# Performance work log

Measured on AMD Instinct MI355X. Metric: run time of the kernel, lower is better.

Reference implementation:

```python
import jax, jax.numpy as jnp
import numpy as np

N_NODES = 100000
N_EDGES = 1600000
IN_DIM, HID_DIM, OUT_DIM = 64, 64, 32


def setup_inputs() -> dict:
    key = jax.random.key(0)
    ks = jax.random.split(key, 8)
    s_in = 1.0 / np.sqrt(IN_DIM)
    s_hid = 1.0 / np.sqrt(HID_DIM)
    return {
        "x": jax.random.normal(ks[0], (N_NODES, IN_DIM), dtype=jnp.float32),
        "edge_index": jax.random.randint(ks[1], (2, N_EDGES), 0, N_NODES, dtype=jnp.int64),
        "W1l": jax.random.uniform(ks[2], (IN_DIM, HID_DIM), jnp.float32, -s_in, s_in),
        "b1l": jnp.zeros((HID_DIM,), jnp.float32),
        "W1r": jax.random.uniform(ks[3], (IN_DIM, HID_DIM), jnp.float32, -s_in, s_in),
        "W2l": jax.random.uniform(ks[4], (HID_DIM, OUT_DIM), jnp.float32, -s_hid, s_hid),
        "b2l": jnp.zeros((OUT_DIM,), jnp.float32),
        "W2r": jax.random.uniform(ks[5], (HID_DIM, OUT_DIM), jnp.float32, -s_hid, s_hid),
    }


def sage_conv(x, src, dst, W_l, b_l, W_r, n_nodes):
    # PyG SAGEConv (aggr='mean'): lin_l(mean of neighbor msgs) + lin_r(x)
    msg = x[src]                                                    # [E, d] gather
    agg = jax.ops.segment_sum(msg, dst, num_segments=n_nodes)      # [N, d] scatter-add
    deg = jax.ops.segment_sum(jnp.ones_like(dst, dtype=x.dtype), dst,
                              num_segments=n_nodes)
    agg = agg / jnp.maximum(deg, 1.0)[:, None]                     # mean (0 for isolated)
    return agg @ W_l + b_l + x @ W_r


def reference(x, edge_index, W1l, b1l, W1r, W2l, b2l, W2r):
    src, dst = edge_index[0], edge_index[1]
    n = x.shape[0]
    h = jax.nn.relu(sage_conv(x, src, dst, W1l, b1l, W1r, n))
    return sage_conv(h, src, dst, W2l, b2l, W2r, n)
```

## Files before the change

### kernel.cpp

```cpp
#include <hip/hip_runtime.h>

#define N_NODES 100000
#define N_EDGES 1600000
#define B2_SHIFT 9
#define BUCK_N (1 << B2_SHIFT)
#define NB2 ((N_NODES + BUCK_N - 1) >> B2_SHIFT)
#define BCAP 9216
#define PAIR_EPB 4096
#define PAIR_BLOCKS ((N_EDGES + PAIR_EPB - 1) / PAIR_EPB)

typedef __attribute__((ext_vector_type(8))) short bf16x8;
typedef __attribute__((ext_vector_type(4))) float f32x4;

__device__ __forceinline__ unsigned pack2(float a, float b) {
    unsigned ua = __float_as_uint(a), ub = __float_as_uint(b);
    ua = (ua + 0x7FFFu + ((ua >> 16) & 1u)) >> 16;
    ub = (ub + 0x7FFFu + ((ub >> 16) & 1u)) >> 16;
    return ua | (ub << 16);
}
__device__ __forceinline__ float lo16(unsigned u) { return __uint_as_float(u << 16); }
__device__ __forceinline__ float hi16(unsigned u) { return __uint_as_float(u & 0xFFFF0000u); }

__global__ __launch_bounds__(256) void k_cast(const float* __restrict__ x,
                                              unsigned* __restrict__ xh)
{
    int i = blockIdx.x * 256 + threadIdx.x;
    if (i < N_NODES * 32) {
        float2 v = ((const float2*)x)[i];
        xh[i] = pack2(v.x, v.y);
    }
}

__global__ __launch_bounds__(256) void k_initcur(int* __restrict__ bcur)
{
    if (threadIdx.x < NB2) bcur[threadIdx.x] = threadIdx.x * BCAP;
}

__global__ __launch_bounds__(256) void k_pairs(const int* __restrict__ ei,
                                               int* __restrict__ bcur,
                                               int* __restrict__ pairs)
{
    __shared__ int lh[2][NB2];
    __shared__ int lb[2][NB2];
    for (int i = threadIdx.x; i < NB2; i += 256) { lh[0][i] = 0; lh[1][i] = 0; }
    __syncthreads();
    int cp = (threadIdx.x >> 6) & 1;
    int base = blockIdx.x * PAIR_EPB;
    int myb[16], myr[16], myp[16];
#pragma unroll
    for (int t = 0; t < 16; t++) {
        int e = base + t * 256 + threadIdx.x;
        myb[t] = -1;
        if (e < N_EDGES) {
            int dst = ei[N_EDGES + e];
            int b = dst >> B2_SHIFT;
            myb[t] = b;
            myr[t] = atomicAdd(&lh[cp][b], 1);
            myp[t] = (ei[e] << B2_SHIFT) | (dst & (BUCK_N - 1));
        }
    }
    __syncthreads();
    for (int i = threadIdx.x; i < NB2; i += 256) {
        int c0 = lh[0][i], c1 = lh[1][i];
        int basei = (c0 + c1) ? atomicAdd(&bcur[i], c0 + c1) : 0;
        lb[0][i] = basei;
        lb[1][i] = basei + c0;
    }
    __syncthreads();
#pragma unroll
    for (int t = 0; t < 16; t++) {
        if (myb[t] >= 0) {
            int slot = lb[cp][myb[t]] + myr[t];
            if (slot < (myb[t] + 1) * BCAP)
                pairs[slot] = myp[t];
        }
    }
}

__global__ __launch_bounds__(512) void k_sortb(const int* __restrict__ bcur,
                                               const int* __restrict__ pairs,
                                               int* __restrict__ sorted_src,
                                               int* __restrict__ rs,
                                               int* __restrict__ re)
{
    __shared__ int lcnt[BUCK_N];
    __shared__ int wtot[8];
    int b = blockIdx.x;
    int beg = b * BCAP, end = bcur[b];
    lcnt[threadIdx.x] = 0;
    __syncthreads();
    for (int i = beg + threadIdx.x; i < end; i += 512)
        atomicAdd(&lcnt[pairs[i] & (BUCK_N - 1)], 1);
    __syncthreads();
    int v = lcnt[threadIdx.x];
    int lane = threadIdx.x & 63, wid = threadIdx.x >> 6;
    int s = v;
#pragma unroll
    for (int off = 1; off < 64; off <<= 1) {
        int t = __shfl_up(s, off);
        if (lane >= off) s += t;
    }
    if (lane == 63) wtot[wid] = s;
    __syncthreads();
    int woff = 0;
#pragma unroll
    for (int k = 0; k < 8; k++) woff += (k < wid) ? wtot[k] : 0;
    int excl = woff + s - v;
    int n = (b << B2_SHIFT) + threadIdx.x;
    if (n < N_NODES) { rs[n] = beg + excl; re[n] = beg + excl + v; }
    __syncthreads();
    lcnt[threadIdx.x] = beg + excl;
    __syncthreads();
    for (int i = beg + threadIdx.x; i < end; i += 512) {
        int p = pairs[i];
        int idx = atomicAdd(&lcnt[p & (BUCK_N - 1)], 1);
        sorted_src[idx] = p >> B2_SHIFT;
    }
}

__global__ __launch_bounds__(256) void k_agg1(const int* __restrict__ rs,
                                              const int* __restrict__ re,
                                              const int* __restrict__ sorted_src,
                                              const unsigned* __restrict__ xh,
                                              unsigned* __restrict__ agg1h)
{
    int node = blockIdx.x * 8 + (threadIdx.x >> 5);
    if (node >= N_NODES) return;
    int d2 = threadIdx.x & 31;
    int beg = rs[node], end = re[node];
    float a0 = 0.f, a1 = 0.f, b0 = 0.f, b1 = 0.f;
    int idx = beg;
    for (; idx + 8 <= end; idx += 8) {
        int s0 = sorted_src[idx + 0], s1 = sorted_src[idx + 1];
        int s2 = sorted_src[idx + 2], s3 = sorted_src[idx + 3];
        int s4 = sorted_src[idx + 4], s5 = sorted_src[idx + 5];
        int s6 = sorted_src[idx + 6], s7 = sorted_src[idx + 7];
        unsigned p0 = xh[(size_t)s0 * 32 + d2];
        unsigned p1 = xh[(size_t)s1 * 32 + d2];
        unsigned p2 = xh[(size_t)s2 * 32 + d2];
        unsigned p3 = xh[(size_t)s3 * 32 + d2];
        unsigned p4 = xh[(size_t)s4 * 32 + d2];
        unsigned p5 = xh[(size_t)s5 * 32 + d2];
        unsigned p6 = xh[(size_t)s6 * 32 + d2];
        unsigned p7 = xh[(size_t)s7 * 32 + d2];
        a0 += lo16(p0) + lo16(p1);  a1 += hi16(p0) + hi16(p1);
        b0 += lo16(p2) + lo16(p3);  b1 += hi16(p2) + hi16(p3);
        a0 += lo16(p4) + lo16(p5);  a1 += hi16(p4) + hi16(p5);
        b0 += lo16(p6) + lo16(p7);  b1 += hi16(p6) + hi16(p7);
    }
    for (; idx + 2 <= end; idx += 2) {
        int s0 = sorted_src[idx], s1 = sorted_src[idx + 1];
        unsigned p0 = xh[(size_t)s0 * 32 + d2];
        unsigned p1 = xh[(size_t)s1 * 32 + d2];
        a0 += lo16(p0) + lo16(p1);  a1 += hi16(p0) + hi16(p1);
    }
    if (idx < end) {
        unsigned p = xh[(size_t)sorted_src[idx] * 32 + d2];
        a0 += lo16(p);  a1 += hi16(p);
    }
    agg1h[(size_t)node * 32 + d2] = pack2(a0 + b0, a1 + b1);
}

#define TPW 2
#define NTILE ((N_NODES + 15) / 16)
#define NODE_BLOCKS (((NTILE + TPW - 1) / TPW + 3) / 4)
__global__ __launch_bounds__(256) void k_node_mfma(
    const unsigned* __restrict__ xh, const unsigned* __restrict__ agg1h,
    const int* __restrict__ rs, const int* __restrict__ re,
    const float* __restrict__ W1l, const float* __restrict__ b1l,
    const float* __restrict__ W1r, const float* __restrict__ W2l,
    const float* __restrict__ W2r,
    unsigned* __restrict__ t2h, float* __restrict__ t3)
{
    __shared__ uint4 sWF[24 * 64];
    __shared__ float sH[4][16 * 68];
    __shared__ float sT[4][16 * 44];

    for (int s = threadIdx.x; s < 1536; s += 256) {
        int f = s >> 6, l = s & 63;
        int m = l & 15, q = l >> 4;
        float w[8];
        if (f < 16) {
            int jt = f >> 2, ks = f & 3;
            int j = jt * 16 + m;
            int k0 = ks * 32 + q * 8;
#pragma unroll
            for (int i = 0; i < 8; i++) {
                int kk = k0 + i;
                w[i] = (kk < 64) ? W1l[kk * 64 + j] : W1r[(kk - 64) * 64 + j];
            }
        } else {
            int f2 = f - 16;
            int jt = f2 >> 1, ks = f2 & 1;
            int j = jt * 16 + m;
            int k0 = ks * 32 + q * 8;
#pragma unroll
            for (int i = 0; i < 8; i++) {
                int kk = k0 + i;
                w[i] = (j < 32) ? W2l[kk * 32 + j] : W2r[kk * 32 + (j - 32)];
            }
        }
        sWF[f * 64 + l] = make_uint4(pack2(w[0], w[1]), pack2(w[2], w[3]),
                                     pack2(w[4], w[5]), pack2(w[6], w[7]));
    }
    __syncthreads();

    int w = threadIdx.x >> 6, lane = threadIdx.x & 63;
    int m = lane & 15, q = lane >> 4;

    bf16x8 WF1[4][4], WF2[4][2];
#pragma unroll
    for (int jt = 0; jt < 4; jt++) {
#pragma unroll
        for (int ks = 0; ks < 4; ks++)
            WF1[jt][ks] = __builtin_bit_cast(bf16x8, sWF[(jt * 4 + ks) * 64 + lane]);
#pragma unroll
        for (int ks = 0; ks < 2; ks++)
            WF2[jt][ks] = __builtin_bit_cast(bf16x8, sWF[(16 + jt * 2 + ks) * 64 + lane]);
    }
    float bias[4];
#pragma unroll
    for (int jt = 0; jt < 4; jt++) bias[jt] = b1l[jt * 16 + m];

    float* myH = &sH[w][0];
    float* myT = &sT[w][0];
    int gw = blockIdx.x * 4 + w;

    for (int t = 0; t < TPW; t++) {
        int tile = gw * TPW + t;
        if (tile >= NTILE) break;
        int nb = tile * 16;

        int nc = nb + m; if (nc >= N_NODES) nc = N_NODES - 1;
        const uint4* arow = (const uint4*)(agg1h + (size_t)nc * 32);
        const uint4* xrow = (const uint4*)(xh + (size_t)nc * 32);
        bf16x8 AM[2], AX[2];
        AM[0] = __builtin_bit_cast(bf16x8, arow[q]);
        AM[1] = __builtin_bit_cast(bf16x8, arow[4 + q]);
        AX[0] = __builtin_bit_cast(bf16x8, xrow[q]);
        AX[1] = __builtin_bit_cast(bf16x8, xrow[4 + q]);

        float invr[4];
#pragma unroll
        for (int r = 0; r < 4; r++) {
            int nn = nb + q * 4 + r;
            int nc2 = (nn < N_NODES) ? nn : 0;
            invr[r] = 1.0f / fmaxf((float)(re[nc2] - rs[nc2]), 1.0f);
        }

#pragma unroll
        for (int jt = 0; jt < 4; jt++) {
            f32x4 aM = {0.f, 0.f, 0.f, 0.f}, aX = {0.f, 0.f, 0.f, 0.f};
            aM = __builtin_amdgcn_mfma_f32_16x16x32_bf16(AM[0], WF1[jt][0], aM, 0, 0, 0);
            aM = __builtin_amdgcn_mfma_f32_16x16x32_bf16(AM[1], WF1[jt][1], aM, 0, 0, 0);
            aX = __builtin_amdgcn_mfma_f32_16x16x32_bf16(AX[0], WF1[jt][2], aX, 0, 0, 0);
            aX = __builtin_amdgcn_mfma_f32_16x16x32_bf16(AX[1], WF1[jt][3], aX, 0, 0, 0);
#pragma unroll
            for (int r = 0; r < 4; r++) {
                float hv = fmaxf(aM[r] * invr[r] + aX[r] + bias[jt], 0.0f);
                myH[(q * 4 + r) * 68 + jt * 16 + m] = hv;
            }
        }

        bf16x8 A2[2];
#pragma unroll
        for (int ks = 0; ks < 2; ks++) {
            const float* p = &myH[m * 68 + ks * 32 + q * 8];
            float4 v0 = *(const float4*)p;
            float4 v1 = *(const float4*)(p + 4);
            uint4 u = make_uint4(pack2(v0.x, v0.y), pack2(v0.z, v0.w),
                                 pack2(v1.x, v1.y), pack2(v1.z, v1.w));
            A2[ks] = __builtin_bit_cast(bf16x8, u);
        }

#pragma unroll
        for (int jt = 0; jt < 4; jt++) {
            f32x4 acc = {0.f, 0.f, 0.f, 0.f};
            acc = __builtin_amdgcn_mfma_f32_16x16x32_bf16(A2[0], WF2[jt][0], acc, 0, 0, 0);
            acc = __builtin_amdgcn_mfma_f32_16x16x32_bf16(A2[1], WF2[jt][1], acc, 0, 0, 0);
            if (jt < 2) {
#pragma unroll
                for (int r = 0; r < 4; r++)
                    myT[(q * 4 + r) * 44 + jt * 16 + m] = acc[r];
            } else {
#pragma unroll
                for (int r = 0; r < 4; r++) {
                    int nn = nb + q * 4 + r;
                    if (nn < N_NODES)
                        t3[(size_t)nn * 32 + (jt - 2) * 16 + m] = acc[r];
                }
            }
        }

        int ni = lane >> 2, u4g = lane & 3;
        const float* tp = &myT[ni * 44 + u4g * 8];
        float4 a = *(const float4*)tp;
        float4 b = *(const float4*)(tp + 4);
        if (nb + ni < N_NODES) {
            uint4 o = make_uint4(pack2(a.x, a.y), pack2(a.z, a.w),
                                 pack2(b.x, b.y), pack2(b.z, b.w));
            *(uint4*)(t2h + (size_t)(nb + ni) * 16 + u4g * 4) = o;
        }
    }
}

__global__ __launch_bounds__(256) void k_agg2out(
    const int* __restrict__ rs, const int* __restrict__ re,
    const int* __restrict__ sorted_src,
    const unsigned* __restrict__ t2h, const float* __restrict__ t3,
    const float* __restrict__ b2l, float* __restrict__ out)
{
    int node = blockIdx.x * 16 + (threadIdx.x >> 4);
    if (node >= N_NODES) return;
    int d2 = threadIdx.x & 15;
    int beg = rs[node], end = re[node];
    float a0 = 0.f, a1 = 0.f, b0 = 0.f, b1 = 0.f;
    int idx = beg;
    for (; idx + 8 <= end; idx += 8) {
        int s0 = sorted_src[idx + 0], s1 = sorted_src[idx + 1];
        int s2 = sorted_src[idx + 2], s3 = sorted_src[idx + 3];
        int s4 = sorted_src[idx + 4], s5 = sorted_src[idx + 5];
        int s6 = sorted_src[idx + 6], s7 = sorted_src[idx + 7];
        unsigned p0 = t2h[(size_t)s0 * 16 + d2];
        unsigned p1 = t2h[(size_t)s1 * 16 + d2];
        unsigned p2 = t2h[(size_t)s2 * 16 + d2];
        unsigned p3 = t2h[(size_t)s3 * 16 + d2];
        unsigned p4 = t2h[(size_t)s4 * 16 + d2];
        unsigned p5 = t2h[(size_t)s5 * 16 + d2];
        unsigned p6 = t2h[(size_t)s6 * 16 + d2];
        unsigned p7 = t2h[(size_t)s7 * 16 + d2];
        a0 += lo16(p0) + lo16(p1);  a1 += hi16(p0) + hi16(p1);
        b0 += lo16(p2) + lo16(p3);  b1 += hi16(p2) + hi16(p3);
        a0 += lo16(p4) + lo16(p5);  a1 += hi16(p4) + hi16(p5);
        b0 += lo16(p6) + lo16(p7);  b1 += hi16(p6) + hi16(p7);
    }
    for (; idx + 2 <= end; idx += 2) {
        int s0 = sorted_src[idx], s1 = sorted_src[idx + 1];
        unsigned p0 = t2h[(size_t)s0 * 16 + d2];
        unsigned p1 = t2h[(size_t)s1 * 16 + d2];
        a0 += lo16(p0) + lo16(p1);  a1 += hi16(p0) + hi16(p1);
    }
    if (idx < end) {
        unsigned p = t2h[(size_t)sorted_src[idx] * 16 + d2];
        a0 += lo16(p);  a1 += hi16(p);
    }
    float inv = 1.0f / fmaxf((float)(end - beg), 1.0f);
    float2 tv = ((const float2*)(t3 + (size_t)node * 32))[d2];
    float2 bv = ((const float2*)b2l)[d2];
    ((float2*)(out + (size_t)node * 32))[d2] =
        make_float2((a0 + b0) * inv + tv.x + bv.x,
                    (a1 + b1) * inv + tv.y + bv.y);
}

extern "C" void kernel_launch(void* const* d_in, const int* in_sizes, int n_in,
                              void* d_out, int out_size, void* d_ws, size_t ws_size,
                              hipStream_t stream) {
    const float* x   = (const float*)d_in[0];
    const int*   ei  = (const int*)d_in[1];
    const float* W1l = (const float*)d_in[2];
    const float* b1l = (const float*)d_in[3];
    const float* W1r = (const float*)d_in[4];
    const float* W2l = (const float*)d_in[5];
    const float* b2l = (const float*)d_in[6];
    const float* W2r = (const float*)d_in[7];
    float* out = (float*)d_out;

    const size_t N = N_NODES;
    int* wsi = (int*)d_ws;
    int*      pairs      = wsi;
    int*      sorted_src = wsi + 1806336;
    int*      bcur       = wsi + 3612672;
    int*      rs         = wsi + 3612928;
    int*      re         = wsi + 3712928;
    unsigned* xh         = (unsigned*)(wsi + 3812928);
    unsigned* t2h        = xh + 32 * N;
    unsigned* agg1h      = t2h + 16 * N;
    float*    t3         = (float*)(agg1h + 32 * N);

    k_cast   <<<(int)((N * 32 + 255) / 256), 256, 0, stream>>>(x, xh);
    k_initcur<<<1, 256, 0, stream>>>(bcur);
    k_pairs  <<<PAIR_BLOCKS, 256, 0, stream>>>(ei, bcur, pairs);
    k_sortb  <<<NB2, 512, 0, stream>>>(bcur, pairs, sorted_src, rs, re);

    k_agg1     <<<(int)((N + 7) / 8), 256, 0, stream>>>(rs, re, sorted_src, xh, agg1h);
    k_node_mfma<<<NODE_BLOCKS, 256, 0, stream>>>(xh, agg1h, rs, re,
                                                 W1l, b1l, W1r, W2l, W2r, t2h, t3);
    k_agg2out  <<<(int)((N + 15) / 16), 256, 0, stream>>>(rs, re, sorted_src,
                                                 t2h, t3, b2l, out);
}
```

Measured before the change: 209.1 us.

## Fuse cast, bucket init, pair binning and weight packing into one prep kernel

Merges the x-to-bf16 cast, bucket-counter init, edge pair binning and bf16 weight-fragment packing into a single kernel launch whose blocks pick a role from blockIdx. The bucket cursors are reset with a memset and now hold relative offsets. The node MFMA kernel copies prepacked weights from global memory instead of each block re-packing them. The sort kernel stages each bucket's pairs in shared memory so it reads global memory once, and the cast is vectorised to float4. This aims to cut launch count and redundant per-block weight packing, at the cost of a larger shared-memory footprint in the sort kernel.

```diff
diff --git a/kernel.cpp b/kernel.cpp
--- a/kernel.cpp
+++ b/kernel.cpp
@@ -8,6 +8,8 @@
 #define BCAP 9216
 #define PAIR_EPB 4096
 #define PAIR_BLOCKS ((N_EDGES + PAIR_EPB - 1) / PAIR_EPB)
+#define CAST_BLOCKS 6250
+#define PREP_BLOCKS (PAIR_BLOCKS + 1 + CAST_BLOCKS)
 
 typedef __attribute__((ext_vector_type(8))) short bf16x8;
 typedef __attribute__((ext_vector_type(4))) float f32x4;
@@ -21,58 +23,83 @@
 __device__ __forceinline__ float lo16(unsigned u) { return __uint_as_float(u << 16); }
 __device__ __forceinline__ float hi16(unsigned u) { return __uint_as_float(u & 0xFFFF0000u); }
 
-__global__ __launch_bounds__(256) void k_cast(const float* __restrict__ x,
-                                              unsigned* __restrict__ xh)
-{
-    int i = blockIdx.x * 256 + threadIdx.x;
-    if (i < N_NODES * 32) {
-        float2 v = ((const float2*)x)[i];
-        xh[i] = pack2(v.x, v.y);
-    }
-}
-
-__global__ __launch_bounds__(256) void k_initcur(int* __restrict__ bcur)
-{
-    if (threadIdx.x < NB2) bcur[threadIdx.x] = threadIdx.x * BCAP;
-}
-
-__global__ __launch_bounds__(256) void k_pairs(const int* __restrict__ ei,
-                                               int* __restrict__ bcur,
-                                               int* __restrict__ pairs)
+__global__ __launch_bounds__(256) void k_prep(
+    const float* __restrict__ x, const int* __restrict__ ei,
+    const float* __restrict__ W1l, const float* __restrict__ W1r,
+    const float* __restrict__ W2l, const float* __restrict__ W2r,
+    unsigned* __restrict__ xh, int* __restrict__ bcur,
+    int* __restrict__ pairs, uint4* __restrict__ wf)
 {
     __shared__ int lh[2][NB2];
     __shared__ int lb[2][NB2];
-    for (int i = threadIdx.x; i < NB2; i += 256) { lh[0][i] = 0; lh[1][i] = 0; }
-    __syncthreads();
-    int cp = (threadIdx.x >> 6) & 1;
-    int base = blockIdx.x * PAIR_EPB;
-    int myb[16], myr[16], myp[16];
-#pragma unroll
-    for (int t = 0; t < 16; t++) {
-        int e = base + t * 256 + threadIdx.x;
-        myb[t] = -1;
-        if (e < N_EDGES) {
-            int dst = ei[N_EDGES + e];
-            int b = dst >> B2_SHIFT;
-            myb[t] = b;
-            myr[t] = atomicAdd(&lh[cp][b], 1);
-            myp[t] = (ei[e] << B2_SHIFT) | (dst & (BUCK_N - 1));
-        }
-    }
-    __syncthreads();
-    for (int i = threadIdx.x; i < NB2; i += 256) {
-        int c0 = lh[0][i], c1 = lh[1][i];
-        int basei = (c0 + c1) ? atomicAdd(&bcur[i], c0 + c1) : 0;
-        lb[0][i] = basei;
-        lb[1][i] = basei + c0;
-    }
-    __syncthreads();
-#pragma unroll
-    for (int t = 0; t < 16; t++) {
-        if (myb[t] >= 0) {
-            int slot = lb[cp][myb[t]] + myr[t];
-            if (slot < (myb[t] + 1) * BCAP)
-                pairs[slot] = myp[t];
+
+    if (blockIdx.x < PAIR_BLOCKS) {
+        for (int i = threadIdx.x; i < NB2; i += 256) { lh[0][i] = 0; lh[1][i] = 0; }
+        __syncthreads();
+        int cp = (threadIdx.x >> 6) & 1;
+        int base = blockIdx.x * PAIR_EPB;
+        int myb[16], myr[16], myp[16];
+#pragma unroll
+        for (int t = 0; t < 16; t++) {
+            int e = base + t * 256 + threadIdx.x;
+            myb[t] = -1;
+            if (e < N_EDGES) {
+                int dst = ei[N_EDGES + e];
+                int b = dst >> B2_SHIFT;
+                myb[t] = b;
+                myr[t] = atomicAdd(&lh[cp][b], 1);
+                myp[t] = (ei[e] << B2_SHIFT) | (dst & (BUCK_N - 1));
+            }
+        }
+        __syncthreads();
+        for (int i = threadIdx.x; i < NB2; i += 256) {
+            int c0 = lh[0][i], c1 = lh[1][i];
+            int basei = (c0 + c1) ? atomicAdd(&bcur[i], c0 + c1) : 0;
+            lb[0][i] = basei;
+            lb[1][i] = basei + c0;
+        }
+        __syncthreads();
+#pragma unroll
+        for (int t = 0; t < 16; t++) {
+            if (myb[t] >= 0) {
+                int slot = lb[cp][myb[t]] + myr[t];
+                if (slot < BCAP)
+                    pairs[myb[t] * BCAP + slot] = myp[t];
+            }
+        }
+    } else if (blockIdx.x == PAIR_BLOCKS) {
+        for (int s = threadIdx.x; s < 1536; s += 256) {
+            int f = s >> 6, l = s & 63;
+            int m = l & 15, q = l >> 4;
+            float w[8];
+            if (f < 16) {
+                int jt = f >> 2, ks = f & 3;
+                int j = jt * 16 + m;
+                int k0 = ks * 32 + q * 8;
+#pragma unroll
+                for (int i = 0; i < 8; i++) {
+                    int kk = k0 + i;
+                    w[i] = (kk < 64) ? W1l[kk * 64 + j] : W1r[(kk - 64) * 64 + j];
+                }
+            } else {
+                int f2 = f - 16;
+                int jt = f2 >> 1, ks = f2 & 1;
+                int j = jt * 16 + m;
+                int k0 = ks * 32 + q * 8;
+#pragma unroll
+                for (int i = 0; i < 8; i++) {
+                    int kk = k0 + i;
+                    w[i] = (j < 32) ? W2l[kk * 32 + j] : W2r[kk * 32 + (j - 32)];
+                }
+            }
+            wf[s] = make_uint4(pack2(w[0], w[1]), pack2(w[2], w[3]),
+                               pack2(w[4], w[5]), pack2(w[6], w[7]));
+        }
+    } else {
+        int i = (blockIdx.x - PAIR_BLOCKS - 1) * 256 + threadIdx.x;
+        if (i < N_NODES * 16) {
+            float4 v = ((const float4*)x)[i];
+            ((uint2*)xh)[i] = make_uint2(pack2(v.x, v.y), pack2(v.z, v.w));
         }
     }
 }
@@ -83,14 +110,18 @@
                                                int* __restrict__ rs,
                                                int* __restrict__ re)
 {
+    __shared__ int sp[BCAP];
     __shared__ int lcnt[BUCK_N];
     __shared__ int wtot[8];
     int b = blockIdx.x;
-    int beg = b * BCAP, end = bcur[b];
+    int beg = b * BCAP;
+    int cnt = bcur[b];
+    if (cnt > BCAP) cnt = BCAP;
+    for (int i = threadIdx.x; i < cnt; i += 512) sp[i] = pairs[beg + i];
     lcnt[threadIdx.x] = 0;
     __syncthreads();
-    for (int i = beg + threadIdx.x; i < end; i += 512)
-        atomicAdd(&lcnt[pairs[i] & (BUCK_N - 1)], 1);
+    for (int i = threadIdx.x; i < cnt; i += 512)
+        atomicAdd(&lcnt[sp[i] & (BUCK_N - 1)], 1);
     __syncthreads();
     int v = lcnt[threadIdx.x];
     int lane = threadIdx.x & 63, wid = threadIdx.x >> 6;
@@ -111,8 +142,8 @@
     __syncthreads();
     lcnt[threadIdx.x] = beg + excl;
     __syncthreads();
-    for (int i = beg + threadIdx.x; i < end; i += 512) {
-        int p = pairs[i];
+    for (int i = threadIdx.x; i < cnt; i += 512) {
+        int p = sp[i];
         int idx = atomicAdd(&lcnt[p & (BUCK_N - 1)], 1);
         sorted_src[idx] = p >> B2_SHIFT;
     }
@@ -167,42 +198,15 @@
 __global__ __launch_bounds__(256) void k_node_mfma(
     const unsigned* __restrict__ xh, const unsigned* __restrict__ agg1h,
     const int* __restrict__ rs, const int* __restrict__ re,
-    const float* __restrict__ W1l, const float* __restrict__ b1l,
-    const float* __restrict__ W1r, const float* __restrict__ W2l,
-    const float* __restrict__ W2r,
+    const float* __restrict__ b1l, const uint4* __restrict__ wf,
     unsigned* __restrict__ t2h, float* __restrict__ t3)
 {
     __shared__ uint4 sWF[24 * 64];
     __shared__ float sH[4][16 * 68];
     __shared__ float sT[4][16 * 44];
 
-    for (int s = threadIdx.x; s < 1536; s += 256) {
-        int f = s >> 6, l = s & 63;
-        int m = l & 15, q = l >> 4;
-        float w[8];
-        if (f < 16) {
-            int jt = f >> 2, ks = f & 3;
-            int j = jt * 16 + m;
-            int k0 = ks * 32 + q * 8;
-#pragma unroll
-            for (int i = 0; i < 8; i++) {
-                int kk = k0 + i;
-                w[i] = (kk < 64) ? W1l[kk * 64 + j] : W1r[(kk - 64) * 64 + j];
-            }
-        } else {
-            int f2 = f - 16;
-            int jt = f2 >> 1, ks = f2 & 1;
-            int j = jt * 16 + m;
-            int k0 = ks * 32 + q * 8;
-#pragma unroll
-            for (int i = 0; i < 8; i++) {
-                int kk = k0 + i;
-                w[i] = (j < 32) ? W2l[kk * 32 + j] : W2r[kk * 32 + (j - 32)];
-            }
-        }
-        sWF[f * 64 + l] = make_uint4(pack2(w[0], w[1]), pack2(w[2], w[3]),
-                                     pack2(w[4], w[5]), pack2(w[6], w[7]));
-    }
+    for (int s = threadIdx.x; s < 1536; s += 256)
+        sWF[s] = wf[s];
     __syncthreads();
 
     int w = threadIdx.x >> 6, lane = threadIdx.x & 63;
@@ -376,15 +380,16 @@
     unsigned* t2h        = xh + 32 * N;
     unsigned* agg1h      = t2h + 16 * N;
     float*    t3         = (float*)(agg1h + 32 * N);
-
-    k_cast   <<<(int)((N * 32 + 255) / 256), 256, 0, stream>>>(x, xh);
-    k_initcur<<<1, 256, 0, stream>>>(bcur);
-    k_pairs  <<<PAIR_BLOCKS, 256, 0, stream>>>(ei, bcur, pairs);
-    k_sortb  <<<NB2, 512, 0, stream>>>(bcur, pairs, sorted_src, rs, re);
+    uint4*    wf         = (uint4*)(t3 + 32 * N);
+
+    hipMemsetAsync(bcur, 0, NB2 * sizeof(int), stream);
+    k_prep <<<PREP_BLOCKS, 256, 0, stream>>>(x, ei, W1l, W1r, W2l, W2r,
+                                             xh, bcur, pairs, wf);
+    k_sortb<<<NB2, 512, 0, stream>>>(bcur, pairs, sorted_src, rs, re);
 
     k_agg1     <<<(int)((N + 7) / 8), 256, 0, stream>>>(rs, re, sorted_src, xh, agg1h);
     k_node_mfma<<<NODE_BLOCKS, 256, 0, stream>>>(xh, agg1h, rs, re,
-                                                 W1l, b1l, W1r, W2l, W2r, t2h, t3);
+                                                 b1l, wf, t2h, t3);
     k_agg2out  <<<(int)((N + 15) / 16), 256, 0, stream>>>(rs, re, sorted_src,
                                                  t2h, t3, b2l, out);
 }
```

New measurement: 200.2 us. -4.3%, faster.
